# Kernel tuning notes

Measured on AMD Instinct MI355X. Metric: run time of the kernel, lower is better.

Reference implementation:

```python
import jax, jax.numpy as jnp
import numpy as np

EPS = 1e-12  # matches torch F.normalize eps


def setup_inputs() -> dict:
    key = jax.random.key(0)
    k1, k2 = jax.random.split(key)
    N, D, K = 262144, 128, 512
    embeddings = jax.random.normal(k1, (N, D), dtype=jnp.float32)
    init_centroids = jax.random.normal(k2, (K, D), dtype=jnp.float32)
    return {"embeddings": embeddings, "init_centroids": init_centroids, "num_iters": 5}


def _kmeans_iter(centroids, embeddings, K):
    # [N, K] similarity, hard assignment by argmax (k-means E-step with dot-product metric)
    dots = jnp.matmul(embeddings, centroids.T)
    assign = jnp.argmax(dots, axis=1)  # [N] int32
    # M-step: per-cluster sum + counts (replaces CPU dict-of-lists + python loop)
    emb_sums = jax.ops.segment_sum(embeddings, assign, num_segments=K)  # [K, D]
    counts = jax.ops.segment_sum(jnp.ones(embeddings.shape[0], dtype=embeddings.dtype),
                                 assign, num_segments=K)  # [K]
    # only update clusters with members (mask = counts > 0), keep old centroid otherwise
    new_c = jnp.where(counts[:, None] > 0,
                      emb_sums / jnp.maximum(counts, 1.0)[:, None],
                      centroids)
    # F.normalize(dim=1, p=2) applied to ALL centroids
    norm = jnp.maximum(jnp.linalg.norm(new_c, axis=1, keepdims=True), EPS)
    return new_c / norm, assign


def reference(embeddings, init_centroids, num_iters):
    K = init_centroids.shape[0]
    centroids = init_centroids
    assign = jnp.zeros(embeddings.shape[0], dtype=jnp.int32)
    for _ in range(num_iters):  # small static iteration count (k-means iters)
        centroids, assign = _kmeans_iter(centroids, embeddings, K)
    return assign, centroids
```

## Files before the change

kernel.cpp:

```cpp
#include <hip/hip_runtime.h>

#define NN 262144
#define DD 128
#define KK 512
#define NITER 5

#define SKH 136

#define SE 132
#define SC 260
#define SS 129

#define DELTA 2e-3f

#define WS_A16_BYTES   (NN * 2)
#define WS_SUMS_OFF    (WS_A16_BYTES)
#define WS_CNTS_OFF    (WS_SUMS_OFF + 2048 * DD * 4)
#define WS_NEEDED      (WS_CNTS_OFF + 2048 * 4)
#define WS_CH_OFF      (WS_SUMS_OFF + NN)
#define WS_CL_OFF      (WS_CH_OFF + KK * DD * 2)
#define WS_EAB3_OFF    (WS_NEEDED)
#define WS_EAB3_BYTES  (NN * DD * 4)
#define WS_NEEDED2     (WS_EAB3_OFF + WS_EAB3_BYTES)

using s8     = __attribute__((ext_vector_type(8))) short;
using f32x4  = __attribute__((ext_vector_type(4))) float;
using f32x16 = __attribute__((ext_vector_type(16))) float;

__device__ __forceinline__ unsigned f2bf(float x) {
    unsigned u = __float_as_uint(x);
    return (u + 0x7fffu + ((u >> 16) & 1u)) >> 16;
}

__device__ __forceinline__ void split4(float4 v, uint2& h, uint2& s) {
    unsigned hx = f2bf(v.x), hy = f2bf(v.y), hz = f2bf(v.z), hw = f2bf(v.w);
    float rx = v.x - __uint_as_float(hx << 16);
    float ry = v.y - __uint_as_float(hy << 16);
    float rz = v.z - __uint_as_float(hz << 16);
    float rw = v.w - __uint_as_float(hw << 16);
    unsigned lx = f2bf(rx), ly = f2bf(ry), lz = f2bf(rz), lw = f2bf(rw);
    h.x = hx | (hy << 16); h.y = hz | (hw << 16);
    s.x = lx | (ly << 16); s.y = lz | (lw << 16);
}

__global__ __launch_bounds__(256) void presplit_e3_kernel(
    const float* __restrict__ E, unsigned short* __restrict__ EAB)
{
    const int u   = blockIdx.x * 4 + (threadIdx.x >> 6);
    const int l   = threadIdx.x & 63;
    const int g32 = u >> 3, ks = u & 7;
    const int row = g32 * 32 + (l & 31);
    const int k0  = ks * 16 + (l >> 5) * 8;
    float4 v0 = *(const float4*)&E[(size_t)row * DD + k0];
    float4 v1 = *(const float4*)&E[(size_t)row * DD + k0 + 4];
    uint2 h0, s0, h1, s1;
    split4(v0, h0, s0); split4(v1, h1, s1);
    size_t base = (size_t)u * 2048 + l * 16;
    *(uint2*)((char*)EAB + base)        = h0;
    *(uint2*)((char*)EAB + base + 8)    = h1;
    *(uint2*)((char*)EAB + base + 1024) = s0;
    *(uint2*)((char*)EAB + base + 1032) = s1;
}

__global__ __launch_bounds__(256) void split_c3_kernel(
    const float* __restrict__ C, unsigned short* __restrict__ CH,
    unsigned short* __restrict__ CL)
{
    int idx = blockIdx.x * 256 + threadIdx.x;
    int col = idx >> 5;
    int k4  = (idx & 31) << 2;
    float4 v = *(const float4*)&C[(size_t)col * DD + k4];
    uint2 h, s;
    split4(v, h, s);
    int unit = (col >> 5) * 8 + (k4 >> 4);
    int lane = (col & 31) + ((k4 >> 3) & 1) * 32;
    int off  = unit * 512 + lane * 8 + (k4 & 7);
    *(uint2*)&CH[off] = h;
    *(uint2*)&CL[off] = s;
}

__global__ __launch_bounds__(256, 2) void assign5_kernel(
    const unsigned short* __restrict__ EAB,
    const unsigned short* __restrict__ CH, const unsigned short* __restrict__ CL,
    int* __restrict__ assignv, unsigned short* __restrict__ assign16,
    unsigned char* __restrict__ flags)
{
    __shared__ char bld[2][32768];

    const int tid = threadIdx.x;
    const int l   = tid & 63;
    const int wid = tid >> 6;
    const int j   = l & 31;
    const int h   = l >> 5;
    const int r0  = blockIdx.x * 128;
    const int g32 = blockIdx.x * 4 + wid;

    const char* Abase = (const char*)EAB + (size_t)g32 * 16384 + l * 16;
    s8 Ah[8], Al[8];
#pragma unroll
    for (int ks = 0; ks < 8; ++ks) {
        Ah[ks] = *(const s8*)(Abase + ks * 2048);
        Al[ks] = *(const s8*)(Abase + ks * 2048 + 1024);
    }

    float bv[16], sv[16];
    int   bk[16];
#pragma unroll
    for (int i = 0; i < 16; ++i) { bv[i] = -3.4e38f; sv[i] = -3.4e38f; bk[i] = 0; }

    {
        uint4 rH[4], rL[4];
#pragma unroll
        for (int p = 0; p < 4; ++p) {
            rH[p] = *(const uint4*)((const char*)CH + (p * 256 + tid) * 16);
            rL[p] = *(const uint4*)((const char*)CL + (p * 256 + tid) * 16);
        }
#pragma unroll
        for (int p = 0; p < 4; ++p) {
            *(uint4*)(bld[0] + (p * 256 + tid) * 16)         = rH[p];
            *(uint4*)(bld[0] + 16384 + (p * 256 + tid) * 16) = rL[p];
        }
    }
    __syncthreads();

#pragma unroll
    for (int hc = 0; hc < 8; ++hc) {
        const int cur = hc & 1, nxt = cur ^ 1;

        uint4 rH[4], rL[4];
        if (hc < 7) {
            const char* srcH = (const char*)CH + (hc + 1) * 16384;
            const char* srcL = (const char*)CL + (hc + 1) * 16384;
#pragma unroll
            for (int p = 0; p < 4; ++p) {
                rH[p] = *(const uint4*)(srcH + (p * 256 + tid) * 16);
                rL[p] = *(const uint4*)(srcL + (p * 256 + tid) * 16);
            }
        }

        f32x16 acc[2];
#pragma unroll
        for (int cfi = 0; cfi < 2; ++cfi)
#pragma unroll
            for (int r = 0; r < 16; ++r) acc[cfi][r] = 0.f;

#pragma unroll
        for (int ks = 0; ks < 8; ++ks) {
#pragma unroll
            for (int cfi = 0; cfi < 2; ++cfi) {
                const int uu = cfi * 8 + ks;
                s8 bh = *(const s8*)(bld[cur] + uu * 1024 + l * 16);
                s8 bl = *(const s8*)(bld[cur] + 16384 + uu * 1024 + l * 16);
                acc[cfi] = __builtin_amdgcn_mfma_f32_32x32x16_bf16(
                    Ah[ks], bh, acc[cfi], 0, 0, 0);
                acc[cfi] = __builtin_amdgcn_mfma_f32_32x32x16_bf16(
                    Ah[ks], bl, acc[cfi], 0, 0, 0);
                acc[cfi] = __builtin_amdgcn_mfma_f32_32x32x16_bf16(
                    Al[ks], bh, acc[cfi], 0, 0, 0);
            }
        }

#pragma unroll
        for (int cfi = 0; cfi < 2; ++cfi) {
            const int kg = hc * 64 + cfi * 32 + j;
#pragma unroll
            for (int r = 0; r < 16; ++r) {
                float v = acc[cfi][r];
                if (v > bv[r]) { sv[r] = bv[r]; bv[r] = v; bk[r] = kg; }
                else           { sv[r] = fmaxf(sv[r], v); }
            }
        }

        if (hc < 7) {
#pragma unroll
            for (int p = 0; p < 4; ++p) {
                *(uint4*)(bld[nxt] + (p * 256 + tid) * 16)         = rH[p];
                *(uint4*)(bld[nxt] + 16384 + (p * 256 + tid) * 16) = rL[p];
            }
            __syncthreads();
        }
    }

#pragma unroll
    for (int r = 0; r < 16; ++r) {
        float v1 = bv[r], v2 = sv[r]; int k1 = bk[r];
#pragma unroll
        for (int m = 1; m <= 16; m <<= 1) {
            float ov = __shfl_xor(v1, m, 64);
            float os = __shfl_xor(v2, m, 64);
            int   ok = __shfl_xor(k1, m, 64);
            if (ov > v1) { v2 = fmaxf(v1, os); v1 = ov; k1 = ok; }
            else         { v2 = fmaxf(v2, ov); }
        }
        bv[r] = v1; sv[r] = v2; bk[r] = k1;
    }

#pragma unroll
    for (int r = 0; r < 16; ++r) {
        if (j == r) {
            int rowg = r0 + wid * 32 + (r & 3) + 8 * (r >> 2) + 4 * h;
            assignv[rowg]  = bk[r];
            assign16[rowg] = (unsigned short)bk[r];
            flags[rowg]    = (bv[r] - sv[r] < DELTA) ? 1 : 0;
        }
    }
}

__global__ __launch_bounds__(256) void split_c_kernel(
    const float* __restrict__ C, unsigned short* __restrict__ CH,
    unsigned short* __restrict__ CL)
{
    int idx = blockIdx.x * 256 + threadIdx.x;
    int col = idx >> 5;
    int k4  = (idx & 31) << 2;
    float4 v = *(const float4*)&C[(size_t)col * DD + k4];
    uint2 h, s;
    split4(v, h, s);
    int group = (col >> 4) * 4 + (k4 >> 5);
    int inner = ((k4 >> 3) & 3) * 16 + (col & 15);
    int off   = group * 512 + inner * 8 + (k4 & 7);
    *(uint2*)&CH[off] = h;
    *(uint2*)&CL[off] = s;
}

__global__ __launch_bounds__(256, 2) void assign_kernel(
    const float* __restrict__ E,
    const unsigned short* __restrict__ CH, const unsigned short* __restrict__ CL,
    int* __restrict__ assignv, unsigned short* __restrict__ assign16,
    unsigned char* __restrict__ flags)
{
    __shared__ unsigned short lds[2 * 128 * SKH];
    unsigned short* EH = lds;
    unsigned short* EL = lds + 128 * SKH;

    const int tid = threadIdx.x;
    const int l   = tid & 63;
    const int wid = tid >> 6;
    const int wr  = wid >> 1;
    const int wc  = wid & 1;
    const int c   = l & 15;
    const int g   = l >> 4;
    const int r0  = blockIdx.x * 128;

#pragma unroll
    for (int it = 0; it < 16; ++it) {
        int idx = it * 256 + tid;
        int row = idx >> 5;
        int k4  = (idx & 31) << 2;
        float4 v = *(const float4*)&E[(size_t)(r0 + row) * DD + k4];
        uint2 h, s;
        split4(v, h, s);
        *(uint2*)&EH[row * SKH + k4] = h;
        *(uint2*)&EL[row * SKH + k4] = s;
    }
    __syncthreads();

    float bv[16], sv[16];
    int   bk[16];
#pragma unroll
    for (int i = 0; i < 16; ++i) { bv[i] = -3.4e38f; sv[i] = -3.4e38f; bk[i] = 0; }

    const int aoff0 = (wr * 64 + c) * SKH + g * 8;
    const int bbase = wc * 16 * 512 + l * 8;

    s8 bh[2][4], bl[2][4];
#pragma unroll
    for (int cf = 0; cf < 4; ++cf) {
        int off = bbase + (cf * 4) * 512;
        bh[0][cf] = *(const s8*)&CH[off];
        bl[0][cf] = *(const s8*)&CL[off];
    }

    f32x4 acc[4][4];

#pragma unroll
    for (int t = 0; t < 16; ++t) {
        const int cc  = t >> 2, kc = t & 3;
        const int cur = t & 1,  nxt = cur ^ 1;

        if (kc == 0) {
#pragma unroll
            for (int rf = 0; rf < 4; ++rf)
#pragma unroll
                for (int cf = 0; cf < 4; ++cf)
                    acc[rf][cf] = (f32x4){0.f, 0.f, 0.f, 0.f};
        }

        if (t < 15) {
            const int t1 = t + 1, cc1 = t1 >> 2, kc1 = t1 & 3;
#pragma unroll
            for (int cf = 0; cf < 4; ++cf) {
                int off = bbase + (cc1 * 32 + cf * 4 + kc1) * 512;
                bh[nxt][cf] = *(const s8*)&CH[off];
                bl[nxt][cf] = *(const s8*)&CL[off];
            }
        }

        s8 ah[4], al[4];
#pragma unroll
        for (int rf = 0; rf < 4; ++rf) {
            int off = aoff0 + rf * 16 * SKH + kc * 32;
            ah[rf] = *(const s8*)&EH[off];
            al[rf] = *(const s8*)&EL[off];
        }

#pragma unroll
        for (int rf = 0; rf < 4; ++rf)
#pragma unroll
            for (int cf = 0; cf < 4; ++cf) {
                acc[rf][cf] = __builtin_amdgcn_mfma_f32_16x16x32_bf16(
                    ah[rf], bh[cur][cf], acc[rf][cf], 0, 0, 0);
                acc[rf][cf] = __builtin_amdgcn_mfma_f32_16x16x32_bf16(
                    ah[rf], bl[cur][cf], acc[rf][cf], 0, 0, 0);
                acc[rf][cf] = __builtin_amdgcn_mfma_f32_16x16x32_bf16(
                    al[rf], bh[cur][cf], acc[rf][cf], 0, 0, 0);
            }

        if (kc == 3) {
            const int kbase = cc * 128 + wc * 64 + c;
#pragma unroll
            for (int rf = 0; rf < 4; ++rf)
#pragma unroll
                for (int i = 0; i < 4; ++i) {
                    const int sidx = rf * 4 + i;
#pragma unroll
                    for (int cf = 0; cf < 4; ++cf) {
                        float v = acc[rf][cf][i];
                        int  kg = kbase + cf * 16;
                        if (v > bv[sidx]) { sv[sidx] = bv[sidx]; bv[sidx] = v; bk[sidx] = kg; }
                        else              { sv[sidx] = fmaxf(sv[sidx], v); }
                    }
                }
        }
    }

#pragma unroll
    for (int s = 0; s < 16; ++s) {
        float v1 = bv[s], v2 = sv[s]; int k1 = bk[s];
#pragma unroll
        for (int m = 1; m <= 8; m <<= 1) {
            float ov = __shfl_xor(v1, m, 64);
            float os = __shfl_xor(v2, m, 64);
            int   ok = __shfl_xor(k1, m, 64);
            if (ov > v1) { v2 = fmaxf(v1, os); v1 = ov; k1 = ok; }
            else         { v2 = fmaxf(v2, ov); }
        }
        bv[s] = v1; sv[s] = v2; bk[s] = k1;
    }

    __syncthreads();
    float* mv = (float*)lds;
    int*   mk = (int*)lds + 256;
    float* ms = (float*)lds + 512;
    if (c == 0) {
#pragma unroll
        for (int rf = 0; rf < 4; ++rf)
#pragma unroll
            for (int i = 0; i < 4; ++i) {
                int row = wr * 64 + rf * 16 + g * 4 + i;
                mv[wc * 128 + row] = bv[rf * 4 + i];
                mk[wc * 128 + row] = bk[rf * 4 + i];
                ms[wc * 128 + row] = sv[rf * 4 + i];
            }
    }
    __syncthreads();
    if (tid < 128) {
        float v1 = mv[tid], v2 = ms[tid]; int k1 = mk[tid];
        float ov = mv[128 + tid], os = ms[128 + tid]; int ok = mk[128 + tid];
        if (ov > v1) { v2 = fmaxf(v1, os); v1 = ov; k1 = ok; }
        else         { v2 = fmaxf(v2, ov); }
        assignv[r0 + tid] = k1;
        assign16[r0 + tid] = (unsigned short)k1;
        flags[r0 + tid] = (v1 - v2 < DELTA) ? 1 : 0;
    }
}

__global__ __launch_bounds__(256) void rescue_kernel(
    const float* __restrict__ E, const float* __restrict__ C,
    const unsigned char* __restrict__ flags,
    int* __restrict__ assignv, unsigned short* __restrict__ assign16)
{
    __shared__ int   rows[128];
    __shared__ int   nf;
    __shared__ float ev[DD];
    __shared__ float rv[4];
    __shared__ int   rk[4];

    const int tid  = threadIdx.x;
    const int base = blockIdx.x * 128;

    if (tid == 0) nf = 0;
    __syncthreads();
    if (tid < 128 && flags[base + tid]) {
        int p = atomicAdd(&nf, 1);
        rows[p] = base + tid;
    }
    __syncthreads();
    const int n = nf;
    if (n == 0) return;

    for (int i = 0; i < n; ++i) {
        const int row = rows[i];
        if (tid < 32)
            *(float4*)&ev[tid * 4] = *(const float4*)&E[(size_t)row * DD + tid * 4];
        __syncthreads();

        float d0 = 0.f, d1 = 0.f;
        for (int q = 0; q < 32; ++q) {
            float4 e4 = *(const float4*)&ev[q * 4];
            float4 c0 = *(const float4*)&C[(size_t)tid * DD + q * 4];
            float4 c1 = *(const float4*)&C[(size_t)(tid + 256) * DD + q * 4];
            d0 = fmaf(e4.x, c0.x, d0); d0 = fmaf(e4.y, c0.y, d0);
            d0 = fmaf(e4.z, c0.z, d0); d0 = fmaf(e4.w, c0.w, d0);
            d1 = fmaf(e4.x, c1.x, d1); d1 = fmaf(e4.y, c1.y, d1);
            d1 = fmaf(e4.z, c1.z, d1); d1 = fmaf(e4.w, c1.w, d1);
        }
        float v = (d0 >= d1) ? d0 : d1;
        int   k = (d0 >= d1) ? tid : tid + 256;
#pragma unroll
        for (int m = 1; m <= 32; m <<= 1) {
            float ov = __shfl_xor(v, m, 64);
            int   ok = __shfl_xor(k, m, 64);
            if (ov > v || (ov == v && ok < k)) { v = ov; k = ok; }
        }
        if ((tid & 63) == 0) { rv[tid >> 6] = v; rk[tid >> 6] = k; }
        __syncthreads();
        if (tid == 0) {
            float bv2 = rv[0]; int bk2 = rk[0];
#pragma unroll
            for (int w = 1; w < 4; ++w)
                if (rv[w] > bv2 || (rv[w] == bv2 && rk[w] < bk2)) { bv2 = rv[w]; bk2 = rk[w]; }
            assignv[row] = bk2;
            assign16[row] = (unsigned short)bk2;
        }
        __syncthreads();
    }
}

__global__ __launch_bounds__(256, 2) void assign_valu_kernel(
    const float* __restrict__ E, const float* __restrict__ C,
    int* __restrict__ assignv, unsigned short* __restrict__ assign16)
{
    __shared__ float smem[32 * SE + 32 * SC];
    float* ET = smem;
    float* CT = smem + 32 * SE;
    float* sval = smem;
    int*   sidx = ((int*)smem) + 32 * SS;

    const int tid = threadIdx.x;
    const int tx  = tid & 31;
    const int ty  = tid >> 5;
    const int r0  = blockIdx.x * 128;

    float bbv = 0.f;
    int   bbk = 0;

    for (int chunk = 0; chunk < 2; ++chunk) {
        const int k0 = chunk * 256;
        float acc[16][8];
#pragma unroll
        for (int i = 0; i < 16; ++i)
#pragma unroll
            for (int j = 0; j < 8; ++j) acc[i][j] = 0.f;

        for (int sub = 0; sub < 4; ++sub) {
            const int d0 = sub * 32;
            __syncthreads();
#pragma unroll
            for (int it = 0; it < 4; ++it) {
                int idx = tid + it * 256;
                int r = idx >> 3, q = idx & 7;
                float4 v = *(const float4*)&E[(r0 + r) * DD + d0 + q * 4];
                ET[(q * 4 + 0) * SE + r] = v.x;
                ET[(q * 4 + 1) * SE + r] = v.y;
                ET[(q * 4 + 2) * SE + r] = v.z;
                ET[(q * 4 + 3) * SE + r] = v.w;
            }
#pragma unroll
            for (int it = 0; it < 8; ++it) {
                int idx = tid + it * 256;
                int k = idx >> 3, q = idx & 7;
                float4 v = *(const float4*)&C[(k0 + k) * DD + d0 + q * 4];
                CT[(q * 4 + 0) * SC + k] = v.x;
                CT[(q * 4 + 1) * SC + k] = v.y;
                CT[(q * 4 + 2) * SC + k] = v.z;
                CT[(q * 4 + 3) * SC + k] = v.w;
            }
            __syncthreads();
#pragma unroll 4
            for (int d = 0; d < 32; ++d) {
                float4 a0 = *(const float4*)&ET[d * SE + ty * 16];
                float4 a1 = *(const float4*)&ET[d * SE + ty * 16 + 4];
                float4 a2 = *(const float4*)&ET[d * SE + ty * 16 + 8];
                float4 a3 = *(const float4*)&ET[d * SE + ty * 16 + 12];
                float4 b0 = *(const float4*)&CT[d * SC + tx * 4];
                float4 b1 = *(const float4*)&CT[d * SC + 128 + tx * 4];
                float ra[16] = {a0.x, a0.y, a0.z, a0.w, a1.x, a1.y, a1.z, a1.w,
                                a2.x, a2.y, a2.z, a2.w, a3.x, a3.y, a3.z, a3.w};
                float rb[8]  = {b0.x, b0.y, b0.z, b0.w, b1.x, b1.y, b1.z, b1.w};
#pragma unroll
                for (int i = 0; i < 16; ++i)
#pragma unroll
                    for (int j = 0; j < 8; ++j)
                        acc[i][j] = fmaf(ra[i], rb[j], acc[i][j]);
            }
        }
        __syncthreads();

#pragma unroll
        for (int i = 0; i < 16; ++i) {
            float bv = acc[i][0]; int bj = 0;
#pragma unroll
            for (int j = 1; j < 8; ++j)
                if (acc[i][j] > bv) { bv = acc[i][j]; bj = j; }
            int row = ty * 16 + i;
            int gk = k0 + ((bj < 4) ? (tx * 4 + bj) : (128 + tx * 4 + (bj - 4)));
            sval[tx * SS + row] = bv;
            sidx[tx * SS + row] = gk;
        }
        __syncthreads();
        if (tid < 128) {
            float bv = sval[tid]; int bi = sidx[tid];
            for (int t = 1; t < 32; ++t) {
                float v = sval[t * SS + tid];
                int   x = sidx[t * SS + tid];
                if (v > bv || (v == bv && x < bi)) { bv = v; bi = x; }
            }
            if (chunk == 0 || bv > bbv || (bv == bbv && bi < bbk)) {
                bbv = bv; bbk = bi;
            }
        }
    }
    if (tid < 128) {
        assignv[r0 + tid] = bbk;
        if (assign16) assign16[r0 + tid] = (unsigned short)bbk;
    }
}

__global__ __launch_bounds__(256) void update_partial_kernel(
    const float* __restrict__ E, const unsigned short* __restrict__ assign16,
    float* __restrict__ ws_sums, int* __restrict__ ws_cnts)
{
    const int b   = blockIdx.x;
    const int k   = b >> 2;
    const int qtr = b & 3;

    __shared__ float acc[4][DD];
    __shared__ int   cnts[4];

    const int tid  = threadIdx.x;
    const int w    = tid >> 6;
    const int lane = tid & 63;

    float a0 = 0.f, a1 = 0.f;
    int cnt = 0;
    const int wbase = qtr * (NN / 4) + w * (NN / 16);

    for (int it = 0; it < (NN / 16) / 512; ++it) {
        const int off = wbase + it * 512;
        uint4 p = *(const uint4*)&assign16[off + lane * 8];
        unsigned v[4] = {p.x, p.y, p.z, p.w};
#pragma unroll
        for (int h = 0; h < 4; ++h) {
            int lo = (int)(v[h] & 0xffffu);
            int hi = (int)(v[h] >> 16);
            unsigned long long mlo = __ballot(lo == k);
            unsigned long long mhi = __ballot(hi == k);
            cnt += (int)__popcll(mlo) + (int)__popcll(mhi);
            while (mlo) {
                int b2 = __ffsll((long long)mlo) - 1; mlo &= mlo - 1;
                int row = off + b2 * 8 + h * 2;
                float2 e = *(const float2*)&E[(size_t)row * DD + lane * 2];
                a0 += e.x; a1 += e.y;
            }
            while (mhi) {
                int b2 = __ffsll((long long)mhi) - 1; mhi &= mhi - 1;
                int row = off + b2 * 8 + h * 2 + 1;
                float2 e = *(const float2*)&E[(size_t)row * DD + lane * 2];
                a0 += e.x; a1 += e.y;
            }
        }
    }
    acc[w][lane * 2]     = a0;
    acc[w][lane * 2 + 1] = a1;
    if (lane == 0) cnts[w] = cnt;
    __syncthreads();
    if (tid < DD)
        ws_sums[(size_t)b * DD + tid] = acc[0][tid] + acc[1][tid] + acc[2][tid] + acc[3][tid];
    if (tid == 0)
        ws_cnts[b] = cnts[0] + cnts[1] + cnts[2] + cnts[3];
}

__global__ __launch_bounds__(128) void update_combine_kernel(
    const float* __restrict__ ws_sums, const int* __restrict__ ws_cnts,
    float* __restrict__ C)
{
    const int k = blockIdx.x, t = threadIdx.x;
    __shared__ float red[2];
    const int w = t >> 6, lane = t & 63;

    float s = ws_sums[(size_t)(4 * k + 0) * DD + t]
            + ws_sums[(size_t)(4 * k + 1) * DD + t]
            + ws_sums[(size_t)(4 * k + 2) * DD + t]
            + ws_sums[(size_t)(4 * k + 3) * DD + t];
    int cnt = ws_cnts[4 * k] + ws_cnts[4 * k + 1] + ws_cnts[4 * k + 2] + ws_cnts[4 * k + 3];
    float m = (cnt > 0) ? s / (float)cnt : C[k * DD + t];

    float sq = m * m;
#pragma unroll
    for (int o = 32; o > 0; o >>= 1) sq += __shfl_down(sq, o, 64);
    if (lane == 0) red[w] = sq;
    __syncthreads();
    float nrm = fmaxf(sqrtf(red[0] + red[1]), 1e-12f);
    C[k * DD + t] = m / nrm;
}

__global__ __launch_bounds__(256) void update_kernel(
    const float* __restrict__ E, const int* __restrict__ assignv,
    float* __restrict__ C)
{
    const int k = blockIdx.x;
    __shared__ float acc[4][DD];
    __shared__ int   cnts[4];
    __shared__ float red[4];

    const int tid  = threadIdx.x;
    const int w    = tid >> 6;
    const int lane = tid & 63;

    float a0 = 0.f, a1 = 0.f;
    int cnt = 0;
    const int per_wave = NN / 4;
    const int base = w * per_wave;

    for (int it = 0; it < per_wave / 256; ++it) {
        const int off = base + it * 256;
        int4 as = *(const int4*)&assignv[off + lane * 4];
        int av[4] = {as.x, as.y, as.z, as.w};
#pragma unroll
        for (int ci = 0; ci < 4; ++ci) {
            unsigned long long m = __ballot(av[ci] == k);
            cnt += (int)__popcll(m);
            while (m) {
                int b = __ffsll((long long)m) - 1;
                m &= m - 1;
                int r = off + b * 4 + ci;
                float2 v = *(const float2*)&E[r * DD + lane * 2];
                a0 += v.x; a1 += v.y;
            }
        }
    }
    acc[w][lane * 2]     = a0;
    acc[w][lane * 2 + 1] = a1;
    if (lane == 0) cnts[w] = cnt;
    __syncthreads();

    float m = 0.f;
    const int ctot = cnts[0] + cnts[1] + cnts[2] + cnts[3];
    if (tid < DD) {
        float s = acc[0][tid] + acc[1][tid] + acc[2][tid] + acc[3][tid];
        m = (ctot > 0) ? s / (float)ctot : C[k * DD + tid];
    }
    float sq = m * m;
#pragma unroll
    for (int o = 32; o > 0; o >>= 1) sq += __shfl_down(sq, o, 64);
    if (lane == 0) red[w] = sq;
    __syncthreads();
    if (tid < DD) {
        float nrm = fmaxf(sqrtf(red[0] + red[1]), 1e-12f);
        C[k * DD + tid] = m / nrm;
    }
}

__global__ void finalize_kernel(float* __restrict__ out)
{
    int i = blockIdx.x * 256 + threadIdx.x;
    if (i < NN) {
        int a = ((const int*)out)[i];
        out[i] = (float)a;
    }
}

extern "C" void kernel_launch(void* const* d_in, const int* in_sizes, int n_in,
                              void* d_out, int out_size, void* d_ws, size_t ws_size,
                              hipStream_t stream)
{
    (void)in_sizes; (void)n_in; (void)out_size;

    const float* E  = (const float*)d_in[0];
    const float* C0 = (const float*)d_in[1];

    float* out     = (float*)d_out;
    float* C       = out + NN;
    int*   assignv = (int*)out;

    const bool fast  = (ws_size >= (size_t)WS_NEEDED);
    const bool fast2 = (ws_size >= (size_t)WS_NEEDED2);
    unsigned short* assign16 = fast ? (unsigned short*)d_ws : nullptr;
    float* ws_sums = fast ? (float*)((char*)d_ws + WS_SUMS_OFF) : nullptr;
    int*   ws_cnts = fast ? (int*)((char*)d_ws + WS_CNTS_OFF) : nullptr;
    unsigned char* flags = fast ? (unsigned char*)d_ws + WS_SUMS_OFF : nullptr;
    unsigned short* CH = fast ? (unsigned short*)((char*)d_ws + WS_CH_OFF) : nullptr;
    unsigned short* CL = fast ? (unsigned short*)((char*)d_ws + WS_CL_OFF) : nullptr;
    unsigned short* EAB = fast2 ? (unsigned short*)((char*)d_ws + WS_EAB3_OFF) : nullptr;

    hipMemcpyAsync(C, C0, (size_t)KK * DD * sizeof(float),
                   hipMemcpyDeviceToDevice, stream);

    if (fast2)
        presplit_e3_kernel<<<16384, 256, 0, stream>>>(E, EAB);

    for (int it = 0; it < NITER; ++it) {
        if (fast2) {
            split_c3_kernel<<<KK * DD / 4 / 256, 256, 0, stream>>>(C, CH, CL);
            assign5_kernel<<<NN / 128, 256, 0, stream>>>(EAB, CH, CL,
                                                         assignv, assign16, flags);
            rescue_kernel<<<NN / 128, 256, 0, stream>>>(E, C, flags, assignv, assign16);
            update_partial_kernel<<<2048, 256, 0, stream>>>(E, assign16, ws_sums, ws_cnts);
            update_combine_kernel<<<KK, 128, 0, stream>>>(ws_sums, ws_cnts, C);
        } else if (fast) {
            split_c_kernel<<<KK * DD / 4 / 256, 256, 0, stream>>>(C, CH, CL);
            assign_kernel<<<NN / 128, 256, 0, stream>>>(E, CH, CL, assignv, assign16, flags);
            rescue_kernel<<<NN / 128, 256, 0, stream>>>(E, C, flags, assignv, assign16);
            update_partial_kernel<<<2048, 256, 0, stream>>>(E, assign16, ws_sums, ws_cnts);
            update_combine_kernel<<<KK, 128, 0, stream>>>(ws_sums, ws_cnts, C);
        } else {
            assign_valu_kernel<<<NN / 128, 256, 0, stream>>>(E, C, assignv, nullptr);
            update_kernel<<<KK, 256, 0, stream>>>(E, assignv, C);
        }
    }
    finalize_kernel<<<(NN + 255) / 256, 256, 0, stream>>>(out);
}
```

Baseline: 1.253 ms.

## Replace update partial kernel with ballot-based per-cluster-group gather accumulation

Adds a new M-step partial kernel in which each block owns a group of 4 clusters and one quarter of the points. It scans the assignment array with wave ballots to find matching rows and accumulates those embedding rows in registers, then reduces across 8 waves in shared memory. This avoids atomics and scatter contention in the per-cluster sums. In exchange every block rereads the full assignment slice, and the embedding loads become gathered row reads.

```diff
diff --git a/kernel.cpp b/kernel.cpp
--- a/kernel.cpp
+++ b/kernel.cpp
@@ -206,6 +206,84 @@
     }
 }
 
+__global__ __launch_bounds__(512) void update_partial2_kernel(
+    const float* __restrict__ E, const unsigned short* __restrict__ assign16,
+    float* __restrict__ ws_sums, int* __restrict__ ws_cnts)
+{
+    const int b   = blockIdx.x;
+    const int kg  = b >> 2;
+    const int qtr = b & 3;
+
+    __shared__ float accl[8][4][DD];
+    __shared__ int   cntl[8][4];
+
+    const int tid  = threadIdx.x;
+    const int w    = tid >> 6;
+    const int lane = tid & 63;
+
+    float a0[4] = {0.f, 0.f, 0.f, 0.f};
+    float a1[4] = {0.f, 0.f, 0.f, 0.f};
+    int   cn[4] = {0, 0, 0, 0};
+
+    const int wbase = qtr * (NN / 4) + w * (NN / 32);
+
+    for (int it = 0; it < (NN / 32) / 512; ++it) {
+        const int off = wbase + it * 512;
+        uint4 p = *(const uint4*)&assign16[off + lane * 8];
+        unsigned v[4] = {p.x, p.y, p.z, p.w};
+#pragma unroll
+        for (int h = 0; h < 4; ++h) {
+            int lo = (int)(v[h] & 0xffffu);
+            int hi = (int)(v[h] >> 16);
+            unsigned long long mlo = __ballot((lo >> 2) == kg);
+            unsigned long long mhi = __ballot((hi >> 2) == kg);
+            while (mlo) {
+                int b2 = __ffsll((long long)mlo) - 1; mlo &= mlo - 1;
+                int c2 = __shfl(lo, b2, 64) & 3;
+                int row = off + b2 * 8 + h * 2;
+                float2 e = *(const float2*)&E[(size_t)row * DD + lane * 2];
+                if      (c2 == 0) { a0[0] += e.x; a1[0] += e.y; ++cn[0]; }
+                else if (c2 == 1) { a0[1] += e.x; a1[1] += e.y; ++cn[1]; }
+                else if (c2 == 2) { a0[2] += e.x; a1[2] += e.y; ++cn[2]; }
+                else              { a0[3] += e.x; a1[3] += e.y; ++cn[3]; }
+            }
+            while (mhi) {
+                int b2 = __ffsll((long long)mhi) - 1; mhi &= mhi - 1;
+                int c2 = __shfl(hi, b2, 64) & 3;
+                int row = off + b2 * 8 + h * 2 + 1;
+                float2 e = *(const float2*)&E[(size_t)row * DD + lane * 2];
+                if      (c2 == 0) { a0[0] += e.x; a1[0] += e.y; ++cn[0]; }
+                else if (c2 == 1) { a0[1] += e.x; a1[1] += e.y; ++cn[1]; }
+                else if (c2 == 2) { a0[2] += e.x; a1[2] += e.y; ++cn[2]; }
+                else              { a0[3] += e.x; a1[3] += e.y; ++cn[3]; }
+            }
+        }
+    }
+
+#pragma unroll
+    for (int c2 = 0; c2 < 4; ++c2) {
+        accl[w][c2][lane * 2]     = a0[c2];
+        accl[w][c2][lane * 2 + 1] = a1[c2];
+    }
+    if (lane == 0) {
+#pragma unroll
+        for (int c2 = 0; c2 < 4; ++c2) cntl[w][c2] = cn[c2];
+    }
+    __syncthreads();
+
+    {
+        const int c2 = tid >> 7, d = tid & 127;
+        float s = accl[0][c2][d] + accl[1][c2][d] + accl[2][c2][d] + accl[3][c2][d]
+                + accl[4][c2][d] + accl[5][c2][d] + accl[6][c2][d] + accl[7][c2][d];
+        ws_sums[(size_t)((kg * 4 + c2) * 4 + qtr) * DD + d] = s;
+    }
+    if (tid < 4) {
+        int c = cntl[0][tid] + cntl[1][tid] + cntl[2][tid] + cntl[3][tid]
+              + cntl[4][tid] + cntl[5][tid] + cntl[6][tid] + cntl[7][tid];
+        ws_cnts[(kg * 4 + tid) * 4 + qtr] = c;
+    }
+}
+
 __global__ __launch_bounds__(256) void split_c_kernel(
     const float* __restrict__ C, unsigned short* __restrict__ CH,
     unsigned short* __restrict__ CL)
@@ -716,7 +794,7 @@
             assign5_kernel<<<NN / 128, 256, 0, stream>>>(EAB, CH, CL,
                                                          assignv, assign16, flags);
             rescue_kernel<<<NN / 128, 256, 0, stream>>>(E, C, flags, assignv, assign16);
-            update_partial_kernel<<<2048, 256, 0, stream>>>(E, assign16, ws_sums, ws_cnts);
+            update_partial2_kernel<<<512, 512, 0, stream>>>(E, assign16, ws_sums, ws_cnts);
             update_combine_kernel<<<KK, 128, 0, stream>>>(ws_sums, ws_cnts, C);
         } else if (fast) {
             split_c_kernel<<<KK * DD / 4 / 256, 256, 0, stream>>>(C, CH, CL);
```

Result: slower. 1.311 ms (+4.6%).

## Rewrite per-cluster partial sum kernel with wave-ballot scanning of assignments

Applied to the files above, without the earlier changes.

Replaces the update partial kernel with a version where each block owns one cluster and one quarter of the points. Each of its 8 waves scans the assignment array with ballots and accumulates only the matching embedding rows into registers, then the waves reduce through shared memory. This avoids atomics and scattered writes, but every block reads the whole quarter of the assignment array, so assignment traffic grows with K. Row gathers are serialized per match.

```diff
diff --git a/kernel.cpp b/kernel.cpp
--- a/kernel.cpp
+++ b/kernel.cpp
@@ -206,6 +206,64 @@
     }
 }
 
+__global__ __launch_bounds__(512) void update_partial3_kernel(
+    const float* __restrict__ E, const unsigned short* __restrict__ assign16,
+    float* __restrict__ ws_sums, int* __restrict__ ws_cnts)
+{
+    const int b   = blockIdx.x;
+    const int k   = b >> 2;
+    const int qtr = b & 3;
+
+    __shared__ float acc[8][DD];
+    __shared__ int   cnts[8];
+
+    const int tid  = threadIdx.x;
+    const int w    = tid >> 6;
+    const int lane = tid & 63;
+
+    float a0 = 0.f, a1 = 0.f;
+    int cnt = 0;
+    const int wbase = qtr * (NN / 4) + w * (NN / 32);
+
+    for (int it = 0; it < (NN / 32) / 512; ++it) {
+        const int off = wbase + it * 512;
+        uint4 p = *(const uint4*)&assign16[off + lane * 8];
+        unsigned v[4] = {p.x, p.y, p.z, p.w};
+#pragma unroll
+        for (int h = 0; h < 4; ++h) {
+            int lo = (int)(v[h] & 0xffffu);
+            int hi = (int)(v[h] >> 16);
+            unsigned long long mlo = __ballot(lo == k);
+            unsigned long long mhi = __ballot(hi == k);
+            cnt += (int)__popcll(mlo) + (int)__popcll(mhi);
+            while (mlo) {
+                int b2 = __ffsll((long long)mlo) - 1; mlo &= mlo - 1;
+                int row = off + b2 * 8 + h * 2;
+                float2 e = *(const float2*)&E[(size_t)row * DD + lane * 2];
+                a0 += e.x; a1 += e.y;
+            }
+            while (mhi) {
+                int b2 = __ffsll((long long)mhi) - 1; mhi &= mhi - 1;
+                int row = off + b2 * 8 + h * 2 + 1;
+                float2 e = *(const float2*)&E[(size_t)row * DD + lane * 2];
+                a0 += e.x; a1 += e.y;
+            }
+        }
+    }
+    acc[w][lane * 2]     = a0;
+    acc[w][lane * 2 + 1] = a1;
+    if (lane == 0) cnts[w] = cnt;
+    __syncthreads();
+    if (tid < DD) {
+        float s = acc[0][tid] + acc[1][tid] + acc[2][tid] + acc[3][tid]
+                + acc[4][tid] + acc[5][tid] + acc[6][tid] + acc[7][tid];
+        ws_sums[(size_t)b * DD + tid] = s;
+    }
+    if (tid == 0)
+        ws_cnts[b] = cnts[0] + cnts[1] + cnts[2] + cnts[3]
+                   + cnts[4] + cnts[5] + cnts[6] + cnts[7];
+}
+
 __global__ __launch_bounds__(256) void split_c_kernel(
     const float* __restrict__ C, unsigned short* __restrict__ CH,
     unsigned short* __restrict__ CL)
@@ -716,7 +774,7 @@
             assign5_kernel<<<NN / 128, 256, 0, stream>>>(EAB, CH, CL,
                                                          assignv, assign16, flags);
             rescue_kernel<<<NN / 128, 256, 0, stream>>>(E, C, flags, assignv, assign16);
-            update_partial_kernel<<<2048, 256, 0, stream>>>(E, assign16, ws_sums, ws_cnts);
+            update_partial3_kernel<<<2048, 512, 0, stream>>>(E, assign16, ws_sums, ws_cnts);
             update_combine_kernel<<<KK, 128, 0, stream>>>(ws_sums, ws_cnts, C);
         } else if (fast) {
             split_c_kernel<<<KK * DD / 4 / 256, 256, 0, stream>>>(C, CH, CL);
```

Result: no change. 1.263 ms (median of 2 runs) (+0.8%).
